# Performance work log

Measured on AMD Instinct MI355X. Metric: run time of the kernel, lower is better.

## Reference

```python
import jax, jax.numpy as jnp
import numpy as np
import math

EMBED_DIM = 512
NUM_CLASSES = 100000
BATCH = 512
MARGIN = 0.5
SCALE = 64.0
EASY_MARGIN = False
COS_M = math.cos(MARGIN)
SIN_M = math.sin(MARGIN)
TH = math.cos(math.pi - MARGIN)
MM = math.sin(math.pi - MARGIN) * MARGIN


def setup_inputs() -> dict:
    key = jax.random.key(0)
    k1, k2, k3 = jax.random.split(key, 3)
    inp = jax.random.normal(k1, (BATCH, EMBED_DIM), dtype=jnp.float32)
    # xavier-uniform init for weight [num_classes, embedding_dim]
    limit = math.sqrt(6.0 / (NUM_CLASSES + EMBED_DIM))
    weight = jax.random.uniform(k2, (NUM_CLASSES, EMBED_DIM), dtype=jnp.float32,
                                minval=-limit, maxval=limit)
    target = jax.random.randint(k3, (BATCH,), 0, NUM_CLASSES, dtype=jnp.int64)
    return {"input": inp, "weight": weight, "target": target}


def _l2_normalize(x, axis, eps=1e-12):
    # matches F.normalize(p=2): x / max(||x||, eps)
    n = jnp.sqrt(jnp.sum(x * x, axis=axis, keepdims=True))
    return x / jnp.maximum(n, eps)


def reference(input, weight, target):
    x = _l2_normalize(input, axis=1)                      # [B, D]
    w = _l2_normalize(weight, axis=1)                     # [C, D]
    cosine = jnp.einsum('bd,cd->bc', x, w)                # [B, C]
    # margin only affects the target logit; compute it per-row (same math as
    # the full-matrix where + one_hot blend in the original).
    cos_t = jnp.take_along_axis(cosine, target[:, None].astype(jnp.int32), axis=1)[:, 0]  # [B]
    sin_t = jnp.sqrt(jnp.clip(1.0 - cos_t * cos_t, 0.0, None))
    phi_t = cos_t * COS_M - sin_t * SIN_M
    if EASY_MARGIN:
        phi_t = jnp.where(cos_t > 0, phi_t, cos_t)
    else:
        phi_t = jnp.where(cos_t > TH, phi_t, cos_t - MM)
    # cross-entropy with scaled logits: logsumexp over modified logits - target logit
    # modified logits differ from `cosine*SCALE` only at the target column.
    rows = jnp.arange(cosine.shape[0])
    logits = cosine.at[rows, target.astype(jnp.int32)].set(phi_t) * SCALE  # [B, C]
    lse = jax.scipy.special.logsumexp(logits, axis=1)     # [B]
    loss = jnp.mean(lse - SCALE * phi_t)
    return loss
```

## Files before the change

kernel.cpp:

```cpp
#include <hip/hip_runtime.h>
#include <math.h>


#define NB 512
#define ND 512
#define NC 100000
#define BK 32
#define NCHUNK 16
#define CT 64
#define REP 64
#define FSCALE 64.0f
#define C_COS_M 0.8775825618903728f
#define C_SIN_M 0.479425538604203f
#define C_TH  (-0.8775825618903728f)
#define C_MM  0.2397127693021015f

#define SWZA(b) ((b) ^ (((b) >> 3) & 48))
#define SWZW(b) ((b) ^ (((b) >> 3) & 112))

typedef __bf16 bf16x8 __attribute__((ext_vector_type(8)));
typedef __bf16 bf16x4 __attribute__((ext_vector_type(4)));
typedef float  f32x4  __attribute__((ext_vector_type(4)));
typedef __attribute__((address_space(1))) unsigned int GU;
typedef __attribute__((address_space(3))) unsigned int LU;

__global__ void pack_x_kernel(const float* __restrict__ x, __bf16* __restrict__ xp) {
  const int b = blockIdx.x;
  const int t = threadIdx.x;
  float4 v = reinterpret_cast<const float4*>(x + (size_t)b * ND)[t];
  float ss = v.x*v.x + v.y*v.y + v.z*v.z + v.w*v.w;
  #pragma unroll
  for (int m = 1; m < 64; m <<= 1) ss += __shfl_xor(ss, m);
  __shared__ float sred[2];
  if ((t & 63) == 0) sred[t >> 6] = ss;
  __syncthreads();
  const float rn = rsqrtf(fmaxf(sred[0] + sred[1], 1e-24f));
  bf16x4 o;
  o[0] = (__bf16)(v.x * rn); o[1] = (__bf16)(v.y * rn);
  o[2] = (__bf16)(v.z * rn); o[3] = (__bf16)(v.w * rn);
  const int k = 4 * t;
  const int chunk = k >> 5;
  const int lb = b * 64 + (k & 31) * 2;
  char* dst = (char*)xp + (size_t)chunk * (NB * BK * 2) + SWZA(lb);
  *reinterpret_cast<bf16x4*>(dst) = o;
}

__global__ void cosphi_kernel(const float* __restrict__ x, const float* __restrict__ w,
                              const int* __restrict__ tgt,
                              float* __restrict__ cos_t, float* __restrict__ phi_t) {
  const int b = blockIdx.x;
  const int lane = threadIdx.x;
  const int t = tgt[b];
  const float4* xr = reinterpret_cast<const float4*>(x + (size_t)b * ND);
  const float4* wr = reinterpret_cast<const float4*>(w + (size_t)t * ND);
  float dp = 0.f, xs = 0.f, ws = 0.f;
  #pragma unroll
  for (int j = 0; j < 2; ++j) {
    float4 xv = xr[lane * 2 + j];
    float4 wv = wr[lane * 2 + j];
    dp += xv.x*wv.x + xv.y*wv.y + xv.z*wv.z + xv.w*wv.w;
    xs += xv.x*xv.x + xv.y*xv.y + xv.z*xv.z + xv.w*xv.w;
    ws += wv.x*wv.x + wv.y*wv.y + wv.z*wv.z + wv.w*wv.w;
  }
  #pragma unroll
  for (int m = 1; m < 64; m <<= 1) {
    dp += __shfl_xor(dp, m);
    xs += __shfl_xor(xs, m);
    ws += __shfl_xor(ws, m);
  }
  if (lane == 0) {
    float c = dp * rsqrtf(fmaxf(xs, 1e-24f)) * rsqrtf(fmaxf(ws, 1e-24f));
    c = fminf(fmaxf(c, -1.f), 1.f);
    float s = sqrtf(fmaxf(1.f - c * c, 0.f));
    float phi = c * C_COS_M - s * C_SIN_M;
    phi = (c > C_TH) ? phi : (c - C_MM);
    cos_t[b] = c;
    phi_t[b] = phi;
  }
}

__global__ __launch_bounds__(512, 4) void gemm_lse_kernel(
    const __bf16* __restrict__ xp, const float* __restrict__ w,
    float* __restrict__ gsum) {
  __shared__ __align__(16) char As[2 * NB * BK * 2];
  __shared__ __align__(16) char Ws[2 * CT * BK * 4];

  const int tid  = threadIdx.x;
  const int wv   = tid >> 6;
  const int lane = tid & 63;
  const int bc   = blockIdx.x * CT;

  const int p_w   = wv * 1024 + lane * 16;
  const int lbw   = SWZW(p_w);
  const int wrow  = min(bc + (lbw >> 7), NC - 1);
  const char* wg  = (const char*)w + (size_t)wrow * (ND * 4) + (lbw & 127);

  const char* ag = (const char*)xp + wv * 1024 + lane * 16;

  {
    char* la = As + wv * 1024;
    #pragma unroll
    for (int j = 0; j < 4; ++j)
      __builtin_amdgcn_global_load_lds((const GU*)(ag + j * 8192),
                                       (LU*)(la + j * 8192), 16, 0, 0);
    __builtin_amdgcn_global_load_lds((const GU*)wg, (LU*)(Ws + wv * 1024), 16, 0, 0);
  }

  const int m_w  = wv * 64;
  const int ra   = lane & 15;
  const int quad = lane >> 4;
  int aoff[4], woff[4];
  #pragma unroll
  for (int rt = 0; rt < 4; ++rt)
    aoff[rt] = SWZA((m_w + rt * 16 + ra) * 64 + quad * 16);
  #pragma unroll
  for (int ct = 0; ct < 4; ++ct)
    woff[ct] = SWZW((ct * 16 + ra) * 128 + quad * 32);

  f32x4 acc[4][4] = {};
  float wsq[4] = {0.f, 0.f, 0.f, 0.f};

  __syncthreads();

  for (int c = 0; c < NCHUNK; ++c) {
    const int cur = c & 1;
    if (c + 1 < NCHUNK) {
      const char* a1 = ag + (size_t)(c + 1) * (NB * BK * 2);
      char* la = As + (cur ^ 1) * (NB * BK * 2) + wv * 1024;
      #pragma unroll
      for (int j = 0; j < 4; ++j)
        __builtin_amdgcn_global_load_lds((const GU*)(a1 + j * 8192),
                                         (LU*)(la + j * 8192), 16, 0, 0);
      __builtin_amdgcn_global_load_lds((const GU*)(wg + (size_t)(c + 1) * 128),
                                       (LU*)(Ws + (cur ^ 1) * 8192 + wv * 1024),
                                       16, 0, 0);
    }

    const char* asb = As + cur * (NB * BK * 2);
    const char* wsb = Ws + cur * 8192;
    bf16x8 af[4];
    #pragma unroll
    for (int rt = 0; rt < 4; ++rt)
      af[rt] = *reinterpret_cast<const bf16x8*>(asb + aoff[rt]);
    #pragma unroll
    for (int ct = 0; ct < 4; ++ct) {
      float4 w0 = *reinterpret_cast<const float4*>(wsb + woff[ct]);
      float4 w1 = *reinterpret_cast<const float4*>(wsb + woff[ct] + 16);
      wsq[ct] += w0.x*w0.x + w0.y*w0.y + w0.z*w0.z + w0.w*w0.w
               + w1.x*w1.x + w1.y*w1.y + w1.z*w1.z + w1.w*w1.w;
      bf16x8 bfr;
      bfr[0] = (__bf16)w0.x; bfr[1] = (__bf16)w0.y;
      bfr[2] = (__bf16)w0.z; bfr[3] = (__bf16)w0.w;
      bfr[4] = (__bf16)w1.x; bfr[5] = (__bf16)w1.y;
      bfr[6] = (__bf16)w1.z; bfr[7] = (__bf16)w1.w;
      #pragma unroll
      for (int rt = 0; rt < 4; ++rt)
        acc[rt][ct] = __builtin_amdgcn_mfma_f32_16x16x32_bf16(af[rt], bfr,
                                                              acc[rt][ct], 0, 0, 0);
    }
    __syncthreads();
  }

  float rnw[4];
  int   vmask[4];
  #pragma unroll
  for (int ct = 0; ct < 4; ++ct) {
    wsq[ct] += __shfl_xor(wsq[ct], 16);
    wsq[ct] += __shfl_xor(wsq[ct], 32);
    rnw[ct]   = rsqrtf(fmaxf(wsq[ct], 1e-24f));
    vmask[ct] = (bc + ct * 16 + ra) < NC;
  }

  float* gs = gsum + (size_t)(blockIdx.x & (REP - 1)) * NB;
  #pragma unroll
  for (int rt = 0; rt < 4; ++rt) {
    #pragma unroll
    for (int rg = 0; rg < 4; ++rg) {
      float es = 0.f;
      #pragma unroll
      for (int ct = 0; ct < 4; ++ct) {
        float cosv = acc[rt][ct][rg] * rnw[ct];
        float e = __expf(fmaf(FSCALE, cosv, -FSCALE));
        es += vmask[ct] ? e : 0.f;
      }
      es += __shfl_xor(es, 1);
      es += __shfl_xor(es, 2);
      es += __shfl_xor(es, 4);
      es += __shfl_xor(es, 8);
      if (ra == 0) {
        atomicAdd(&gs[m_w + rt * 16 + quad * 4 + rg], es);
      }
    }
  }
}

__global__ void finalize_kernel(const float* __restrict__ gsum,
                                const float* __restrict__ cos_t,
                                const float* __restrict__ phi_t,
                                float* __restrict__ out) {
  const int b = threadIdx.x;
  float s = 0.f;
  #pragma unroll 8
  for (int r = 0; r < REP; ++r) s += gsum[r * NB + b];
  const float c = cos_t[b];
  const float p = phi_t[b];
  float corr = s - __expf(fmaf(FSCALE, c, -FSCALE))
                 + __expf(fmaf(FSCALE, p, -FSCALE));
  corr = fmaxf(corr, 1e-38f);
  float lb = FSCALE + logf(corr) - FSCALE * p;
  #pragma unroll
  for (int m = 1; m < 64; m <<= 1) lb += __shfl_xor(lb, m);
  __shared__ float pr[8];
  if ((b & 63) == 0) pr[b >> 6] = lb;
  __syncthreads();
  if (b == 0) {
    float tot = 0.f;
    #pragma unroll
    for (int j = 0; j < 8; ++j) tot += pr[j];
    out[0] = tot * (1.0f / NB);
  }
}

extern "C" void kernel_launch(void* const* d_in, const int* in_sizes, int n_in,
                              void* d_out, int out_size, void* d_ws, size_t ws_size,
                              hipStream_t stream) {
  const float* x  = (const float*)d_in[0];
  const float* w  = (const float*)d_in[1];
  const int* tgt  = (const int*)d_in[2];
  float* out      = (float*)d_out;

  __bf16* xp   = (__bf16*)d_ws;
  float* gsum  = (float*)((char*)d_ws + (size_t)NB * ND * 2);
  float* cos_t = gsum + (size_t)REP * NB;
  float* phi_t = cos_t + NB;

  hipMemsetAsync(gsum, 0, (size_t)REP * NB * sizeof(float), stream);
  pack_x_kernel<<<NB, 128, 0, stream>>>(x, xp);
  cosphi_kernel<<<NB, 64, 0, stream>>>(x, w, tgt, cos_t, phi_t);
  const int nblk = (NC + CT - 1) / CT;
  gemm_lse_kernel<<<nblk, 512, 0, stream>>>(xp, w, gsum);
  finalize_kernel<<<1, 512, 0, stream>>>(gsum, cos_t, phi_t, out);
}
```

Before: 381.9 us.

## Pre-normalize and pack weight to bf16 in a separate pass before GEMM

Adds a prep kernel that L2-normalizes each weight row, converts it to bf16 and writes it in the swizzled tile layout the GEMM expects. The GEMM then loads half the bytes per tile into LDS and drops the in-loop fp32-to-bf16 conversion and the squared-norm accumulation. The cost is an extra full pass over the 200MB fp32 weight plus a 100MB bf16 write and a second read of it. The old kernel is kept as a fallback when the workspace is too small.

```diff
diff --git a/kernel.cpp b/kernel.cpp
--- a/kernel.cpp
+++ b/kernel.cpp
@@ -8,6 +8,7 @@
 #define BK 32
 #define NCHUNK 16
 #define CT 64
+#define NTILE 1563
 #define REP 64
 #define FSCALE 64.0f
 #define C_COS_M 0.8775825618903728f
@@ -45,6 +46,35 @@
   *reinterpret_cast<bf16x4*>(dst) = o;
 }
 
+__global__ void prep_w_kernel(const float* __restrict__ w, __bf16* __restrict__ wp) {
+  const int row  = blockIdx.x * 4 + (threadIdx.x >> 6);
+  const int lane = threadIdx.x & 63;
+  if (row >= NTILE * CT) return;
+  const int srow = min(row, NC - 1);
+  const float4* src = reinterpret_cast<const float4*>(w + (size_t)srow * ND);
+  float4 v0 = src[lane * 2];
+  float4 v1 = src[lane * 2 + 1];
+  float ss = v0.x*v0.x + v0.y*v0.y + v0.z*v0.z + v0.w*v0.w
+           + v1.x*v1.x + v1.y*v1.y + v1.z*v1.z + v1.w*v1.w;
+  #pragma unroll
+  for (int m = 1; m < 64; m <<= 1) ss += __shfl_xor(ss, m);
+  float rn = rsqrtf(fmaxf(ss, 1e-24f));
+  if (row >= NC) rn = 0.f;
+  const int tile = row >> 6;
+  const int r64  = row & 63;
+  char* base = (char*)wp + (size_t)tile * (NCHUNK * 4096);
+  #pragma unroll
+  for (int j = 0; j < 2; ++j) {
+    const float4 v = j ? v1 : v0;
+    bf16x4 o;
+    o[0] = (__bf16)(v.x * rn); o[1] = (__bf16)(v.y * rn);
+    o[2] = (__bf16)(v.z * rn); o[3] = (__bf16)(v.w * rn);
+    const int k  = lane * 8 + j * 4;
+    const int lb = r64 * 64 + (k & 31) * 2;
+    *reinterpret_cast<bf16x4*>(base + (k >> 5) * 4096 + SWZA(lb)) = o;
+  }
+}
+
 __global__ void cosphi_kernel(const float* __restrict__ x, const float* __restrict__ w,
                               const int* __restrict__ tgt,
                               float* __restrict__ cos_t, float* __restrict__ phi_t) {
@@ -80,23 +110,119 @@
 }
 
 __global__ __launch_bounds__(512, 4) void gemm_lse_kernel(
+    const __bf16* __restrict__ xp, const __bf16* __restrict__ wp,
+    float* __restrict__ gsum) {
+  __shared__ __align__(16) char As[2 * NB * BK * 2];
+  __shared__ __align__(16) char Ws[2 * CT * BK * 2];
+
+  const int tid  = threadIdx.x;
+  const int wv   = tid >> 6;
+  const int lane = tid & 63;
+  const int bc   = blockIdx.x * CT;
+
+  const char* ag = (const char*)xp + wv * 1024 + lane * 16;
+  const char* wg = (const char*)wp + (size_t)blockIdx.x * (NCHUNK * 4096)
+                   + wv * 1024 + lane * 16;
+
+  {
+    char* la = As + wv * 1024;
+    #pragma unroll
+    for (int j = 0; j < 4; ++j)
+      __builtin_amdgcn_global_load_lds((const GU*)(ag + j * 8192),
+                                       (LU*)(la + j * 8192), 16, 0, 0);
+    if (wv < 4)
+      __builtin_amdgcn_global_load_lds((const GU*)wg, (LU*)(Ws + wv * 1024),
+                                       16, 0, 0);
+  }
+
+  const int m_w  = wv * 64;
+  const int ra   = lane & 15;
+  const int quad = lane >> 4;
+  int aoff[4], boff[4];
+  #pragma unroll
+  for (int rt = 0; rt < 4; ++rt)
+    aoff[rt] = SWZA((m_w + rt * 16 + ra) * 64 + quad * 16);
+  #pragma unroll
+  for (int ct = 0; ct < 4; ++ct)
+    boff[ct] = SWZA((ct * 16 + ra) * 64 + quad * 16);
+
+  f32x4 acc[4][4] = {};
+
+  __syncthreads();
+
+  for (int c = 0; c < NCHUNK; ++c) {
+    const int cur = c & 1;
+    if (c + 1 < NCHUNK) {
+      const char* a1 = ag + (size_t)(c + 1) * (NB * BK * 2);
+      char* la = As + (cur ^ 1) * (NB * BK * 2) + wv * 1024;
+      #pragma unroll
+      for (int j = 0; j < 4; ++j)
+        __builtin_amdgcn_global_load_lds((const GU*)(a1 + j * 8192),
+                                         (LU*)(la + j * 8192), 16, 0, 0);
+      if (wv < 4)
+        __builtin_amdgcn_global_load_lds((const GU*)(wg + (size_t)(c + 1) * 4096),
+                                         (LU*)(Ws + (cur ^ 1) * 4096 + wv * 1024),
+                                         16, 0, 0);
+    }
+
+    const char* asb = As + cur * (NB * BK * 2);
+    const char* wsb = Ws + cur * 4096;
+    bf16x8 af[4], bfr[4];
+    #pragma unroll
+    for (int rt = 0; rt < 4; ++rt)
+      af[rt] = *reinterpret_cast<const bf16x8*>(asb + aoff[rt]);
+    #pragma unroll
+    for (int ct = 0; ct < 4; ++ct)
+      bfr[ct] = *reinterpret_cast<const bf16x8*>(wsb + boff[ct]);
+    #pragma unroll
+    for (int rt = 0; rt < 4; ++rt)
+      #pragma unroll
+      for (int ct = 0; ct < 4; ++ct)
+        acc[rt][ct] = __builtin_amdgcn_mfma_f32_16x16x32_bf16(af[rt], bfr[ct],
+                                                              acc[rt][ct], 0, 0, 0);
+    __syncthreads();
+  }
+
+  int vmask[4];
+  #pragma unroll
+  for (int ct = 0; ct < 4; ++ct)
+    vmask[ct] = (bc + ct * 16 + ra) < NC;
+  float* gs = gsum + (size_t)(blockIdx.x & (REP - 1)) * NB;
+  #pragma unroll
+  for (int rt = 0; rt < 4; ++rt) {
+    #pragma unroll
+    for (int rg = 0; rg < 4; ++rg) {
+      float es = 0.f;
+      #pragma unroll
+      for (int ct = 0; ct < 4; ++ct) {
+        float e = __expf(fmaf(FSCALE, acc[rt][ct][rg], -FSCALE));
+        es += vmask[ct] ? e : 0.f;
+      }
+      es += __shfl_xor(es, 1);
+      es += __shfl_xor(es, 2);
+      es += __shfl_xor(es, 4);
+      es += __shfl_xor(es, 8);
+      if (ra == 0) {
+        atomicAdd(&gs[m_w + rt * 16 + quad * 4 + rg], es);
+      }
+    }
+  }
+}
+
+__global__ __launch_bounds__(512, 4) void gemm_lse_fb(
     const __bf16* __restrict__ xp, const float* __restrict__ w,
     float* __restrict__ gsum) {
   __shared__ __align__(16) char As[2 * NB * BK * 2];
   __shared__ __align__(16) char Ws[2 * CT * BK * 4];
-
   const int tid  = threadIdx.x;
   const int wv   = tid >> 6;
   const int lane = tid & 63;
   const int bc   = blockIdx.x * CT;
-
-  const int p_w   = wv * 1024 + lane * 16;
-  const int lbw   = SWZW(p_w);
-  const int wrow  = min(bc + (lbw >> 7), NC - 1);
-  const char* wg  = (const char*)w + (size_t)wrow * (ND * 4) + (lbw & 127);
-
+  const int p_w  = wv * 1024 + lane * 16;
+  const int lbw  = SWZW(p_w);
+  const int wrow = min(bc + (lbw >> 7), NC - 1);
+  const char* wg = (const char*)w + (size_t)wrow * (ND * 4) + (lbw & 127);
   const char* ag = (const char*)xp + wv * 1024 + lane * 16;
-
   {
     char* la = As + wv * 1024;
     #pragma unroll
@@ -105,9 +231,8 @@
                                        (LU*)(la + j * 8192), 16, 0, 0);
     __builtin_amdgcn_global_load_lds((const GU*)wg, (LU*)(Ws + wv * 1024), 16, 0, 0);
   }
-
-  const int m_w  = wv * 64;
-  const int ra   = lane & 15;
+  const int m_w = wv * 64;
+  const int ra = lane & 15;
   const int quad = lane >> 4;
   int aoff[4], woff[4];
   #pragma unroll
@@ -116,12 +241,9 @@
   #pragma unroll
   for (int ct = 0; ct < 4; ++ct)
     woff[ct] = SWZW((ct * 16 + ra) * 128 + quad * 32);
-
   f32x4 acc[4][4] = {};
   float wsq[4] = {0.f, 0.f, 0.f, 0.f};
-
   __syncthreads();
-
   for (int c = 0; c < NCHUNK; ++c) {
     const int cur = c & 1;
     if (c + 1 < NCHUNK) {
@@ -135,7 +257,6 @@
                                        (LU*)(Ws + (cur ^ 1) * 8192 + wv * 1024),
                                        16, 0, 0);
     }
-
     const char* asb = As + cur * (NB * BK * 2);
     const char* wsb = Ws + cur * 8192;
     bf16x8 af[4];
@@ -160,17 +281,15 @@
     }
     __syncthreads();
   }
-
   float rnw[4];
-  int   vmask[4];
+  int vmask[4];
   #pragma unroll
   for (int ct = 0; ct < 4; ++ct) {
     wsq[ct] += __shfl_xor(wsq[ct], 16);
     wsq[ct] += __shfl_xor(wsq[ct], 32);
-    rnw[ct]   = rsqrtf(fmaxf(wsq[ct], 1e-24f));
+    rnw[ct] = rsqrtf(fmaxf(wsq[ct], 1e-24f));
     vmask[ct] = (bc + ct * 16 + ra) < NC;
   }
-
   float* gs = gsum + (size_t)(blockIdx.x & (REP - 1)) * NB;
   #pragma unroll
   for (int rt = 0; rt < 4; ++rt) {
@@ -187,9 +306,7 @@
       es += __shfl_xor(es, 2);
       es += __shfl_xor(es, 4);
       es += __shfl_xor(es, 8);
-      if (ra == 0) {
-        atomicAdd(&gs[m_w + rt * 16 + quad * 4 + rg], es);
-      }
+      if (ra == 0) atomicAdd(&gs[m_w + rt * 16 + quad * 4 + rg], es);
     }
   }
 }
@@ -233,11 +350,18 @@
   float* gsum  = (float*)((char*)d_ws + (size_t)NB * ND * 2);
   float* cos_t = gsum + (size_t)REP * NB;
   float* phi_t = cos_t + NB;
+  const size_t WPOFF   = 1 << 20;
+  const size_t WPBYTES = (size_t)NTILE * NCHUNK * 4096;
+  __bf16* wp = (__bf16*)((char*)d_ws + WPOFF);
 
   hipMemsetAsync(gsum, 0, (size_t)REP * NB * sizeof(float), stream);
   pack_x_kernel<<<NB, 128, 0, stream>>>(x, xp);
   cosphi_kernel<<<NB, 64, 0, stream>>>(x, w, tgt, cos_t, phi_t);
-  const int nblk = (NC + CT - 1) / CT;
-  gemm_lse_kernel<<<nblk, 512, 0, stream>>>(xp, w, gsum);
+  if (ws_size >= WPOFF + WPBYTES) {
+    prep_w_kernel<<<(NTILE * CT) / 4, 256, 0, stream>>>(w, wp);
+    gemm_lse_kernel<<<NTILE, 512, 0, stream>>>(xp, wp, gsum);
+  } else {
+    gemm_lse_fb<<<NTILE, 512, 0, stream>>>(xp, w, gsum);
+  }
   finalize_kernel<<<1, 512, 0, stream>>>(gsum, cos_t, phi_t, out);
 }
```

Result: no change. 389.1 us (+1.9%).
